# Performance work log

Measured on AMD Instinct MI355X. Metric: run time of the kernel, lower is better.

Reference implementation:

```python
import jax, jax.numpy as jnp
import numpy as np

B, S, H, DH, D, FD, FU = 4, 256, 12, 64, 768, 2048, 2048


def setup_inputs() -> dict:
    key = jax.random.key(0)
    ks = jax.random.split(key, 12)
    s = 0.02  # typical init scale for weights
    return {
        "resid_pre": jax.random.normal(ks[0], (B, S, D), jnp.float32),
        "ln_scale": jax.random.uniform(ks[1], (B, S, 1), jnp.float32, 0.5, 2.0),
        "probs": jax.nn.softmax(jax.random.normal(ks[2], (B, H, S, S), jnp.float32), axis=-1),
        "W_O": jax.random.normal(ks[3], (H, DH, D), jnp.float32) * s,
        "W_V": jax.random.normal(ks[4], (H, D, DH), jnp.float32) * s,
        "enc_W": jax.random.normal(ks[5], (FD, D), jnp.float32) * s,
        "enc_b": jax.random.normal(ks[6], (FD,), jnp.float32) * s,
        "b_dec": jax.random.normal(ks[7], (D,), jnp.float32) * s,
        "up_dec_W": jax.random.normal(ks[8], (D, FU), jnp.float32) * s,
        "up_b_dec": jax.random.normal(ks[9], (D,), jnp.float32) * s,
        "pruned_features": jax.random.normal(ks[10], (B, S, FU), jnp.float32),
        "connection_mask": jax.random.randint(ks[11], (FD, FU), 0, 2, jnp.int32),
    }


def reference(resid_pre, ln_scale, probs, W_O, W_V, enc_W, enc_b, b_dec,
              up_dec_W, up_b_dec, pruned_features, connection_mask):
    # W_OV: [h, d_model(in), d_model(out)]
    W_OV = jnp.einsum('hko,hmk->hmo', W_O, W_V)
    mask = connection_mask.astype(resid_pre.dtype)

    # --- initial contributions ---
    act_ln = resid_pre / ln_scale                                  # [b,s,d]
    pre_moving = jnp.einsum('bsi,hio,fo->bshf', act_ln, W_OV, enc_W)  # [b,s,h,f_down]
    approx = jnp.einsum('bhqk,bkhf->bqf', probs, pre_moving)       # [b,q,f_down]

    # --- pruned contributions (one upstream AE) ---
    virtual = jnp.einsum('fo,hio,iu->hfu', enc_W, W_OV, up_dec_W) * mask[None]
    up_ln = pruned_features / ln_scale                             # [b,k,f_up]
    post_ov = jnp.einsum('bku,hfu->bhkf', up_ln, virtual)          # [b,h,k,f_down]
    approx = approx + jnp.einsum('bhqk,bhkf->bqf', probs, post_ov)

    # --- bias terms ---
    approx = approx + enc_b[None, None] - (enc_W @ b_dec)[None, None]
    ub_ln = up_b_dec[None, None] / ln_scale                        # [b,s,d]
    ub_post = jnp.einsum('hmd,bsm->bsd', W_OV, ub_ln)              # attn path through OV
    approx = approx + jnp.einsum('fd,bsd->bsf', enc_W, ub_post)
    return approx
```

## Files before the change

kernel.cpp:

```cpp
#include <hip/hip_runtime.h>
#include <hip/hip_bf16.h>
#include <stdint.h>

typedef __bf16 bf16;
typedef __bf16 bf16x8 __attribute__((ext_vector_type(8)));
typedef __bf16 bf16x4 __attribute__((ext_vector_type(4)));
typedef float f32x4 __attribute__((ext_vector_type(4)));

#define AS1 __attribute__((address_space(1)))
#define AS3 __attribute__((address_space(3)))


__device__ __forceinline__ void gld16(const bf16* g, bf16* l) {
  __builtin_amdgcn_global_load_lds((AS1 void*)g, (AS3 void*)l, 16, 0, 0);
}

__global__ void k_sentinel(float* __restrict__ out) {
  int i = blockIdx.x * 256 + threadIdx.x;
  if (i < 2097152) out[i] = 1048576.0f;
}


__global__ void k_invln(const float* __restrict__ ln, float* __restrict__ invln) {
  int i = blockIdx.x * 256 + threadIdx.x;
  if (i < 1024) invln[i] = 1.0f / ln[i];
}

__global__ void k_cast4(const float* __restrict__ s, bf16* __restrict__ d, int n4) {
  int i = blockIdx.x * 256 + threadIdx.x;
  if (i < n4) {
    float4 v = *(const float4*)(s + (long)i * 4);
    bf16x4 o;
    o[0] = (bf16)v.x; o[1] = (bf16)v.y; o[2] = (bf16)v.z; o[3] = (bf16)v.w;
    *(bf16x4*)(d + (long)i * 4) = o;
  }
}

__global__ void k_maskb(const int* __restrict__ m, bf16* __restrict__ d, int n4) {
  int i = blockIdx.x * 256 + threadIdx.x;
  if (i < n4) {
    int4 v = *(const int4*)(m + (long)i * 4);
    bf16x4 o;
    o[0] = (bf16)(float)v.x; o[1] = (bf16)(float)v.y;
    o[2] = (bf16)(float)v.z; o[3] = (bf16)(float)v.w;
    *(bf16x4*)(d + (long)i * 4) = o;
  }
}

__global__ void k_probsT(const float* __restrict__ probs, bf16* __restrict__ pT) {
  int i = blockIdx.x * 256 + threadIdx.x;
  if (i < 786432) {
    long idx = (long)i * 4;
    int s  = (int)(idx & 255);
    int q  = (int)((idx >> 8) & 255);
    int hb = (int)(idx >> 16);
    int h = hb % 12, b = hb / 12;
    float4 v = *(const float4*)(probs + idx);
    bf16x4 o;
    o[0] = (bf16)v.x; o[1] = (bf16)v.y; o[2] = (bf16)v.z; o[3] = (bf16)v.w;
    *(bf16x4*)(pT + (long)b * 786432 + (long)q * 3072 + h * 256 + s) = o;
  }
}

__global__ void k_WO(const float* __restrict__ W_O, bf16* __restrict__ WOb) {
  int i = blockIdx.x * 256 + threadIdx.x;
  int o = i % 768, r = (i / 768) & 127, h = i / (768 * 128);
  WOb[i] = (r < 64) ? (bf16)W_O[(long)(h * 64 + r) * 768 + o] : (bf16)0.0f;
}

__global__ void k_WVtT(const float* __restrict__ wv, bf16* __restrict__ WVt) {
  __shared__ float tile[32][33];
  int h = blockIdx.z;
  int k0 = blockIdx.x * 32;
  int i0 = blockIdx.y * 32;
  int lane = threadIdx.x & 31, rg = threadIdx.x >> 5;
  if (k0 < 64) {
    for (int r = rg; r < 32; r += 8)
      tile[r][lane] = wv[((long)(h * 768 + i0 + r)) * 64 + k0 + lane];
    __syncthreads();
    for (int r = rg; r < 32; r += 8)
      WVt[((long)h * 128 + k0 + r) * 768 + i0 + lane] = (bf16)tile[lane][r];
  } else {
    for (int r = rg; r < 32; r += 8)
      WVt[((long)h * 128 + k0 + r) * 768 + i0 + lane] = (bf16)0.0f;
  }
}

__global__ void k_WOt(const float* __restrict__ wo, bf16* __restrict__ W_Ot) {
  __shared__ float tile[32][33];
  int h = blockIdx.z;
  int k0 = blockIdx.x * 32;
  int o0 = blockIdx.y * 32;
  int lane = threadIdx.x & 31, rg = threadIdx.x >> 5;
  for (int r = rg; r < 32; r += 8)
    tile[r][lane] = wo[((long)(h * 64 + k0 + r)) * 768 + o0 + lane];
  __syncthreads();
  for (int r = rg; r < 32; r += 8)
    W_Ot[((long)(h * 768 + o0 + r)) * 64 + k0 + lane] = (bf16)tile[lane][r];
}

__global__ void k_updWtT(const float* __restrict__ u, bf16* __restrict__ d) {
  __shared__ float tile[32][33];
  int u0 = blockIdx.x * 32;
  int i0 = blockIdx.y * 32;
  int lane = threadIdx.x & 31, rg = threadIdx.x >> 5;
  for (int r = rg; r < 32; r += 8)
    tile[r][lane] = u[((long)(i0 + r)) * 2048 + u0 + lane];
  __syncthreads();
  for (int r = rg; r < 32; r += 8)
    d[((long)(u0 + r)) * 768 + i0 + lane] = (bf16)tile[lane][r];
}

__global__ void k_Xb(const float* __restrict__ resid, const float* __restrict__ invln,
                     bf16* __restrict__ Xb) {
  int i = blockIdx.x * 256 + threadIdx.x;
  if (i < 196608) {
    long idx = (long)i * 4;
    float il = invln[idx / 768];
    float4 v = *(const float4*)(resid + idx);
    bf16x4 o;
    o[0] = (bf16)(v.x * il); o[1] = (bf16)(v.y * il);
    o[2] = (bf16)(v.z * il); o[3] = (bf16)(v.w * il);
    *(bf16x4*)(Xb + idx) = o;
  }
}

__global__ void k_UtT(const float* __restrict__ pr, const float* __restrict__ invln,
                      bf16* __restrict__ Ut) {
  __shared__ float tile[32][33];
  int b = blockIdx.z, u0 = blockIdx.x * 32, s0 = blockIdx.y * 32;
  int lane = threadIdx.x & 31, rg = threadIdx.x >> 5;
  for (int r = rg; r < 32; r += 8) {
    int s = s0 + r;
    tile[r][lane] = pr[((long)(b * 256 + s)) * 2048 + u0 + lane] * invln[b * 256 + s];
  }
  __syncthreads();
  for (int r = rg; r < 32; r += 8)
    Ut[((long)b * 2048 + u0 + r) * 256 + s0 + lane] = (bf16)tile[lane][r];
}

__global__ void k_append(const bf16* __restrict__ encWb, bf16* __restrict__ Bt, long ldb) {
  int i = blockIdx.x * 256 + threadIdx.x;
  if (i < 196608) {
    long idx = (long)i * 8;
    int f = (int)(idx / 768), d = (int)(idx % 768);
    *(bf16x8*)(Bt + (long)f * ldb + d) = *(const bf16x8*)(encWb + idx);
  }
}

__global__ void k_sred(const float* __restrict__ Sp, bf16* __restrict__ dst, long ldd) {
  int i = blockIdx.x * 256 + threadIdx.x;
  if (i < 196608) {
    long idx = (long)i * 4;
    int m = (int)(idx / 768), o = (int)(idx % 768);
    float4 v = *(const float4*)(Sp + idx);
    float4 a = *(const float4*)(Sp + 786432 + idx);
    float4 b = *(const float4*)(Sp + 2 * 786432 + idx);
    float4 c = *(const float4*)(Sp + 3 * 786432 + idx);
    v.x += a.x + b.x + c.x; v.y += a.y + b.y + c.y;
    v.z += a.z + b.z + c.z; v.w += a.w + b.w + c.w;
    bf16x4 ov;
    ov[0] = (bf16)v.x; ov[1] = (bf16)v.y; ov[2] = (bf16)v.z; ov[3] = (bf16)v.w;
    *(bf16x4*)(dst + (long)m * ldd + o) = ov;
  }
}


__device__ __forceinline__ float blk_reduce(float s) {
  __shared__ float red[256];
  red[threadIdx.x] = s; __syncthreads();
  for (int o = 128; o > 0; o >>= 1) {
    if ((int)threadIdx.x < o) red[threadIdx.x] += red[threadIdx.x + o];
    __syncthreads();
  }
  float r = red[0]; __syncthreads();
  return r;
}

__global__ void k_bias_t(const float* __restrict__ W_V, const float* __restrict__ up_b,
                         float* __restrict__ t_hk) {
  int j = blockIdx.x, h = j >> 6, k = j & 63;
  float s = 0.f;
  for (int m = threadIdx.x; m < 768; m += 256)
    s += W_V[((long)(h * 768 + m)) * 64 + k] * up_b[m];
  float r = blk_reduce(s);
  if (threadIdx.x == 0) t_hk[j] = r;
}

__global__ void k_bias_w(const float* __restrict__ W_O, const float* __restrict__ t_hk,
                         float* __restrict__ w) {
  int d = blockIdx.x;
  float s = 0.f;
  for (int j = threadIdx.x; j < 768; j += 256)
    s += W_O[(long)j * 768 + d] * t_hk[j];
  float r = blk_reduce(s);
  if (threadIdx.x == 0) w[d] = r;
}

__global__ void k_bias_c(const float* __restrict__ enc_W, const float* __restrict__ enc_b,
                         const float* __restrict__ b_dec, const float* __restrict__ w,
                         float* __restrict__ c0, float* __restrict__ c1) {
  int f = blockIdx.x;
  float s0 = 0.f, s1 = 0.f;
  for (int d = threadIdx.x; d < 768; d += 256) {
    float e = enc_W[(long)f * 768 + d];
    s0 += e * b_dec[d];
    s1 += e * w[d];
  }
  float r0 = blk_reduce(s0);
  float r1 = blk_reduce(s1);
  if (threadIdx.x == 0) { c0[f] = enc_b[f] - r0; c1[f] = r1; }
}

__global__ __launch_bounds__(256)
void gemm_bt(const bf16* __restrict__ A, const bf16* __restrict__ B, void* __restrict__ Cv,
             int M, int N, int K,
             long lda, long ldb, long ldc,
             int batchH,
             long sa_b, long sa_h, long sb_b, long sb_h, long sc_b, long sc_h,
             int mode, int kChunk,
             const bf16* __restrict__ mask, long mask_ld)
{
  __shared__ __align__(16) bf16 Asm[128 * 64];
  __shared__ __align__(16) bf16 Bsm[128 * 64];

  const int t = threadIdx.x;

  const int nbx = gridDim.x, nby = gridDim.y;
  const int nxy = nbx * nby;
  int orig = blockIdx.x + nbx * blockIdx.y;
  int qq = nxy >> 3, rr = nxy & 7;
  int xcd = orig & 7, lid = orig >> 3;
  int swz = (xcd < rr) ? (xcd * (qq + 1) + lid)
                       : (rr * (qq + 1) + (xcd - rr) * qq + lid);
  const int m0 = (swz % nby) * 128;
  const int n0 = (swz / nby) * 128;

  long aoff, boff, coff;
  int k0, k1;
  if (mode == 4) {
    int z = blockIdx.z;
    int bb = z / batchH, kc = z - bb * batchH;
    aoff = (long)bb * sa_b;
    boff = (long)bb * sb_b;
    coff = (long)bb * sc_b + (long)kc * sc_h;
    k0 = kc * kChunk; k1 = k0 + kChunk; if (k1 > K) k1 = K;
  } else if (mode >= 2) {
    int z = blockIdx.z;
    aoff = 0; boff = 0;
    coff = (long)z * (long)M * ldc;
    k0 = z * kChunk; k1 = k0 + kChunk; if (k1 > K) k1 = K;
  } else {
    int z = blockIdx.z;
    int bb = z / batchH, hh = z - bb * batchH;
    aoff = (long)bb * sa_b + (long)hh * sa_h;
    boff = (long)bb * sb_b + (long)hh * sb_h;
    coff = (long)bb * sc_b + (long)hh * sc_h;
    k0 = 0; k1 = K;
  }

  const bf16* Ab = A + aoff + (long)m0 * lda;
  const bf16* Bb = B + boff + (long)n0 * ldb;

  const int r0 = t >> 3;
  const int g8 = t & 7;

  const int L = t & 63, w = t >> 6;
  const int wm = (w & 1) * 64, wn = (w >> 1) * 64;
  const int r16 = L & 15, q = L >> 4;

  f32x4 acc[4][4];
#pragma unroll
  for (int i = 0; i < 4; i++)
#pragma unroll
    for (int j = 0; j < 4; j++) acc[i][j] = (f32x4){0.f, 0.f, 0.f, 0.f};

  for (int kt = k0; kt < k1; kt += 64) {
#pragma unroll
    for (int j = 0; j < 4; j++) {
      int row = j * 32 + r0;
      int sc = ((g8 ^ (row & 7)) << 3);
      gld16(Ab + (long)row * lda + (kt + sc), &Asm[j * 2048 + t * 8]);
      gld16(Bb + (long)row * ldb + (kt + sc), &Bsm[j * 2048 + t * 8]);
    }
    __syncthreads();

#pragma unroll
    for (int h2 = 0; h2 < 2; h2++) {
      bf16x8 af[4], bfr[4];
#pragma unroll
      for (int i = 0; i < 4; i++) {
        int ra = wm + i * 16 + r16;
        af[i]  = *(const bf16x8*)&Asm[ra * 64 + ((((h2 << 2) + q) ^ (ra & 7)) << 3)];
        int rb = wn + i * 16 + r16;
        bfr[i] = *(const bf16x8*)&Bsm[rb * 64 + ((((h2 << 2) + q) ^ (rb & 7)) << 3)];
      }
#pragma unroll
      for (int mi = 0; mi < 4; mi++)
#pragma unroll
        for (int ni = 0; ni < 4; ni++)
          acc[mi][ni] = __builtin_amdgcn_mfma_f32_16x16x32_bf16(af[mi], bfr[ni], acc[mi][ni], 0, 0, 0);
    }
    __syncthreads();
  }

  if (mode >= 2) {
    float* C = (float*)Cv;
#pragma unroll
    for (int mi = 0; mi < 4; mi++)
#pragma unroll
      for (int ni = 0; ni < 4; ni++)
#pragma unroll
        for (int r = 0; r < 4; r++) {
          int gm = m0 + wm + mi * 16 + q * 4 + r;
          int gn = n0 + wn + ni * 16 + r16;
          long idx = coff + (long)gm * ldc + gn;
          float v = acc[mi][ni][r];
          if (mode == 3) v += C[idx];
          C[idx] = v;
        }
  } else {
    bf16* C = (bf16*)Cv;
#pragma unroll
    for (int mi = 0; mi < 4; mi++)
#pragma unroll
      for (int ni = 0; ni < 4; ni++)
#pragma unroll
        for (int r = 0; r < 4; r++) {
          int gm = m0 + wm + mi * 16 + q * 4 + r;
          int gn = n0 + wn + ni * 16 + r16;
          float v = acc[mi][ni][r];
          if (mode == 1) v *= (float)mask[(long)gm * mask_ld + gn];
          C[coff + (long)gm * ldc + gn] = (bf16)v;
        }
  }
}

__global__ __launch_bounds__(512, 2)
void gemm_fp2(const bf16* __restrict__ A, const bf16* __restrict__ B,
              float* __restrict__ C,
              int M, int N, int K, long lda, long ldb, long ldc,
              int mode, int kChunk)
{
  __shared__ __align__(16) bf16 SM[2][2][16384];

  const int t = threadIdx.x;

  const int nz = gridDim.z;
  int fid = blockIdx.x + gridDim.x * (blockIdx.y + gridDim.y * blockIdx.z);
  const int z  = fid % nz;
  const int t2 = fid / nz;
  const int m0 = (t2 >> 3) * 256;
  const int n0 = (t2 & 7) * 256;

  const long coff = (long)z * (long)M * ldc;
  int k0 = z * kChunk, k1 = k0 + kChunk; if (k1 > K) k1 = K;
  const int NT = (k1 > k0) ? (k1 - k0) >> 6 : 0;

  const bf16* Ab = A + (long)m0 * lda + k0;
  const bf16* Bb = B + (long)n0 * ldb + k0;

  const int sr = t >> 3;
  const int g8 = t & 7;

  const int L = t & 63, w = t >> 6;
  const int wm = (w & 1) * 128;
  const int wn = (w >> 1) * 64;
  const int r16 = L & 15, q = L >> 4;

  f32x4 acc[8][4];
#pragma unroll
  for (int i = 0; i < 8; i++)
#pragma unroll
    for (int j = 0; j < 4; j++) acc[i][j] = (f32x4){0.f, 0.f, 0.f, 0.f};

  auto stage = [&](int tt, int buf) {
    const bf16* Ap = Ab + (long)tt * 64;
    const bf16* Bp = Bb + (long)tt * 64;
#pragma unroll
    for (int j = 0; j < 4; j++) {
      int row = j * 64 + sr;
      int sc = ((g8 ^ (row & 7)) << 3);
      gld16(Ap + (long)row * lda + sc, &SM[buf][0][j * 4096 + t * 8]);
    }
#pragma unroll
    for (int j = 0; j < 4; j++) {
      int row = j * 64 + sr;
      int sc = ((g8 ^ (row & 7)) << 3);
      gld16(Bp + (long)row * ldb + sc, &SM[buf][1][j * 4096 + t * 8]);
    }
  };

  if (NT >= 1) stage(0, 0);

  for (int tt = 0; tt < NT; tt++) {
    if (tt + 1 < NT) {
      stage(tt + 1, (tt + 1) & 1);
      asm volatile("s_waitcnt vmcnt(8)" ::: "memory");
    } else {
      asm volatile("s_waitcnt vmcnt(0)" ::: "memory");
    }
    __builtin_amdgcn_s_barrier();

    const bf16* As = &SM[tt & 1][0][0];
    const bf16* Bs = &SM[tt & 1][1][0];
#pragma unroll
    for (int h2 = 0; h2 < 2; h2++) {
      bf16x8 af[8], bfr[4];
#pragma unroll
      for (int i = 0; i < 8; i++) {
        int ra = wm + i * 16 + r16;
        af[i]  = *(const bf16x8*)&As[ra * 64 + ((((h2 << 2) + q) ^ (ra & 7)) << 3)];
      }
#pragma unroll
      for (int i = 0; i < 4; i++) {
        int rb = wn + i * 16 + r16;
        bfr[i] = *(const bf16x8*)&Bs[rb * 64 + ((((h2 << 2) + q) ^ (rb & 7)) << 3)];
      }
#pragma unroll
      for (int mi = 0; mi < 8; mi++)
#pragma unroll
        for (int ni = 0; ni < 4; ni++)
          acc[mi][ni] = __builtin_amdgcn_mfma_f32_16x16x32_bf16(af[mi], bfr[ni], acc[mi][ni], 0, 0, 0);
    }
    __builtin_amdgcn_s_barrier();
  }

#pragma unroll
  for (int mi = 0; mi < 8; mi++)
#pragma unroll
    for (int ni = 0; ni < 4; ni++)
#pragma unroll
      for (int r = 0; r < 4; r++) {
        int gm = m0 + wm + mi * 16 + q * 4 + r;
        int gn = n0 + wn + ni * 16 + r16;
        long idx = coff + (long)gm * ldc + gn;
        float v = acc[mi][ni][r];
        if (mode == 3) v += C[idx];
        C[idx] = v;
      }
}

__global__ void k_out(const float* __restrict__ Cp, const float* __restrict__ c0,
                      const float* __restrict__ c1, const float* __restrict__ invln,
                      float* __restrict__ out, int nsplit) {
  int i4 = blockIdx.x * 256 + threadIdx.x;
  long i = (long)i4 * 4;
  int n = (int)(i & 2047), m = (int)(i >> 11);
  float4 v = *(const float4*)(Cp + i);
  for (int z = 1; z < nsplit; z++) {
    float4 u = *(const float4*)(Cp + i + (long)z * 2097152);
    v.x += u.x; v.y += u.y; v.z += u.z; v.w += u.w;
  }
  float il = invln[m];
  float4 a = *(const float4*)(c0 + n);
  float4 b = *(const float4*)(c1 + n);
  v.x += a.x + b.x * il;
  v.y += a.y + b.y * il;
  v.z += a.z + b.z * il;
  v.w += a.w + b.w * il;
  *(float4*)(out + i) = v;
}


extern "C" void kernel_launch(void* const* d_in, const int* in_sizes, int n_in,
                              void* d_out, int out_size, void* d_ws, size_t ws_size,
                              hipStream_t stream) {
  (void)out_size;
  float* out = (float*)d_out;

  int iresid = -1, iln = -1, iprobs = -1, iencb = -1, ipruned = -1, imask = -1;
  int iwo = -1, iwv = -1, iencw = -1, iupdw = -1, ibdec = -1, iupb = -1;
  for (int i = 0; i < n_in; i++) {
    switch (in_sizes[i]) {
      case 786432:  iresid  = i; break;
      case 1024:    iln     = i; break;
      case 3145728: iprobs  = i; break;
      case 2048:    iencb   = i; break;
      case 2097152: ipruned = i; break;
      case 4194304: imask   = i; break;
      case 589824:  if (iwo   < 0) iwo   = i; else iwv   = i; break;
      case 1572864: if (iencw < 0) iencw = i; else iupdw = i; break;
      case 768:     if (ibdec < 0) ibdec = i; else iupb  = i; break;
      default: break;
    }
  }
  bool ok = n_in == 12 && iresid >= 0 && iln >= 0 && iprobs >= 0 && iencb >= 0 &&
            ipruned >= 0 && imask >= 0 && iwo >= 0 && iwv >= 0 && iencw >= 0 &&
            iupdw >= 0 && ibdec >= 0 && iupb >= 0;
  if (!ok) { k_sentinel<<<8192, 256, 0, stream>>>(out); return; }

  const float* resid = (const float*)d_in[iresid];
  const float* lns   = (const float*)d_in[iln];
  const float* probs = (const float*)d_in[iprobs];
  const float* W_O   = (const float*)d_in[iwo];
  const float* W_V   = (const float*)d_in[iwv];
  const float* enc_W = (const float*)d_in[iencw];
  const float* enc_b = (const float*)d_in[iencb];
  const float* b_dec = (const float*)d_in[ibdec];
  const float* updW  = (const float*)d_in[iupdw];
  const float* up_b  = (const float*)d_in[iupb];
  const float* pruned= (const float*)d_in[ipruned];
  const int*   cmask = (const int*)d_in[imask];

  auto pad = [](size_t b) -> size_t { return (b + 255) & ~(size_t)255; };
  const size_t prepB = pad(2359296) + pad(2359296) + pad(3145728) + pad(1572864) +
                       pad(3145728) + pad(1179648) + pad(3145728) + pad(18874368) +
                       pad(12582912);
  const size_t persB = pad(6291456) + pad(4194304) + pad(6291456) + pad(6291456) +
                       pad(8388608) + pad(4096) + pad(3072) + pad(3072) +
                       pad(8192) + pad(8192);
  auto needB = [&](int g, int ns) -> size_t {
    size_t cp = (size_t)ns * 8388608;
    size_t ov = prepB > cp ? prepB : cp;
    long KA = (long)g * 2048 + 768;
    size_t ab = pad((size_t)1024 * KA * 2) + pad((size_t)2048 * KA * 2);
    return ov + persB + ab + (2ull << 20);
  };
  const int cgs[14] = {12, 12, 12, 6, 6, 4, 3, 2, 2, 1, 1, 1, 1, 1};
  const int cns[14] = { 8,  4, 2, 8, 4, 4, 4, 4, 2, 8, 4, 2, 2, 1};
  int gs = 0, nsplit = 0;
  for (int ci = 0; ci < 14; ci++) {
    if (needB(cgs[ci], cns[ci]) <= ws_size) { gs = cgs[ci]; nsplit = cns[ci]; break; }
  }
  if (gs == 0) { gs = 1; nsplit = 1; }

  const long KA = (long)gs * 2048 + 768;

  char* p = (char*)d_ws;
  auto alloc = [&](size_t bytes) -> char* {
    char* r = p; p += (bytes + 255) & ~(size_t)255; return r;
  };
  char* overlayBase = p;
  bf16*  WOb    = (bf16*)alloc(12ull * 128 * 768 * 2);
  bf16*  WVt    = (bf16*)alloc(12ull * 128 * 768 * 2);
  bf16*  updWt  = (bf16*)alloc(2048ull * 768 * 2);
  bf16*  Xb     = (bf16*)alloc(1024ull * 768 * 2);
  bf16*  encWb  = (bf16*)alloc(2048ull * 768 * 2);
  bf16*  W_Ot   = (bf16*)alloc(12ull * 768 * 64 * 2);
  bf16*  T1     = (bf16*)alloc(12ull * 1024 * 128 * 2);
  bf16*  T3     = (bf16*)alloc(4ull * 768 * 3072 * 2);
  float* Sp     = (float*)alloc(4ull * 1024 * 768 * 4);
  {
    size_t used = (size_t)(p - overlayBase);
    size_t cp = (size_t)nsplit * 8388608;
    p = overlayBase + (used > cp ? used : cp);
  }
  float* Cpart  = (float*)overlayBase;
  bf16*  G_t    = (bf16*)alloc(12ull * 2048 * 128 * 2);
  bf16*  Ut     = (bf16*)alloc(4ull * 2048 * 256 * 2);
  bf16*  E1     = (bf16*)alloc(12ull * 2048 * 128 * 2);
  bf16*  probsT = (bf16*)alloc(4ull * 256 * 3072 * 2);
  bf16*  maskb  = (bf16*)alloc(2048ull * 2048 * 2);
  float* invln  = (float*)alloc(1024 * 4);
  float* t_hk   = (float*)alloc(768 * 4);
  float* wv     = (float*)alloc(768 * 4);
  float* c0     = (float*)alloc(2048 * 4);
  float* c1     = (float*)alloc(2048 * 4);
  bf16*  A_g    = (bf16*)alloc((size_t)1024 * KA * 2);
  bf16*  B_g    = (bf16*)alloc((size_t)2048 * KA * 2);

  k_invln<<<4, 256, 0, stream>>>(lns, invln);
  k_cast4<<<1536, 256, 0, stream>>>(enc_W, encWb, 393216);
  k_probsT<<<3072, 256, 0, stream>>>(probs, probsT);
  k_maskb<<<4096, 256, 0, stream>>>(cmask, maskb, 1048576);
  k_WO<<<4608, 256, 0, stream>>>(W_O, WOb);
  k_WVtT<<<dim3(4, 24, 12), 256, 0, stream>>>(W_V, WVt);
  k_WOt<<<dim3(2, 24, 12), 256, 0, stream>>>(W_O, W_Ot);
  k_updWtT<<<dim3(64, 24), 256, 0, stream>>>(updW, updWt);
  k_Xb<<<768, 256, 0, stream>>>(resid, invln, Xb);
  k_UtT<<<dim3(64, 8, 4), 256, 0, stream>>>(pruned, invln, Ut);
  k_bias_t<<<768, 256, 0, stream>>>(W_V, up_b, t_hk);
  k_bias_w<<<768, 256, 0, stream>>>(W_O, t_hk, wv);
  k_bias_c<<<2048, 256, 0, stream>>>(enc_W, enc_b, b_dec, wv, c0, c1);

  gemm_bt<<<dim3(1, 16, 24), 256, 0, stream>>>(
      encWb, WOb, E1, 2048, 128, 768,
      768, 768, 128, 12,
      (long)(updWt - encWb), 0,
      (long)(WVt - WOb), (long)128 * 768,
      (long)(G_t - E1), (long)2048 * 128,
      0, 0, nullptr, 0);

  gemm_bt<<<dim3(1, 8, 12), 256, 0, stream>>>(
      Xb, WVt, T1, 1024, 128, 768,
      768, 768, 128, 12,
      0, 0, 0, (long)128 * 768, 0, (long)1024 * 128,
      0, 0, nullptr, 0);

  gemm_bt<<<dim3(2, 6, 48), 256, 0, stream>>>(
      W_Ot, T1, T3, 768, 256, 64,
      64, 128, 3072, 12,
      0, (long)768 * 64, (long)256 * 128, (long)1024 * 128, 2359296, 256,
      0, 0, nullptr, 0);

  gemm_bt<<<dim3(6, 2, 16), 256, 0, stream>>>(
      probsT, T3, Sp, 256, 768, 3072,
      3072, 3072, 768, 4,
      786432, 0, 2359296, 0, 196608, 786432,
      4, 768, nullptr, 0);

  k_sred<<<768, 256, 0, stream>>>(Sp, A_g + (long)gs * 2048, KA);

  k_append<<<768, 256, 0, stream>>>(encWb, B_g + (long)gs * 2048, KA);

  for (int g = 0; g < 12 / gs; g++) {
    gemm_bt<<<dim3(16, 16, gs), 256, 0, stream>>>(
        E1 + (long)g * gs * 2048 * 128, G_t + (long)g * gs * 2048 * 128, B_g,
        2048, 2048, 64,
        128, 128, KA, gs,
        0, (long)2048 * 128, 0, (long)2048 * 128, 0, 2048,
        1, 0, maskb, 2048);

    gemm_bt<<<dim3(16, 2, 4 * gs), 256, 0, stream>>>(
        probsT + (long)g * gs * 256, Ut, A_g,
        256, 2048, 256,
        3072, 256, KA, gs,
        786432, 256, (long)2048 * 256, 0, 256 * KA, 2048,
        0, 0, nullptr, 0);

    int Kthis = (g == 0) ? (int)KA : gs * 2048;
    int kc = ((Kthis / nsplit + 63) / 64) * 64;
    gemm_fp2<<<dim3(8, 4, nsplit), 512, 0, stream>>>(
        A_g, B_g, Cpart,
        1024, 2048, Kthis,
        KA, KA, 2048,
        (g == 0) ? 2 : 3, kc);
  }

  k_out<<<2048, 256, 0, stream>>>(Cpart, c0, c1, invln, out, nsplit);
}
```

Before: 450.6 us.

## Merge prep kernels into two launches and retile split-K GEMM to smaller tiles

Ten elementwise and transpose preprocessing kernels are folded into two block-range-dispatched kernels, and the append copy is folded into the prep kernel, writing enc_W straight into B_g. This cuts kernel launch and tail overhead. The main split-K GEMM moves from 256x256 tiles with K-step 64 to 128x256 tiles with K-step 32, with less LDS and launch bounds allowing 4 blocks per CU, and the grid doubles in the M direction. Smaller tiles raise occupancy and block count but lower data reuse per tile and add more barriers per unit of K.

```diff
diff --git a/kernel.cpp b/kernel.cpp
--- a/kernel.cpp
+++ b/kernel.cpp
@@ -20,131 +20,109 @@
   if (i < 2097152) out[i] = 1048576.0f;
 }
 
-
-__global__ void k_invln(const float* __restrict__ ln, float* __restrict__ invln) {
-  int i = blockIdx.x * 256 + threadIdx.x;
-  if (i < 1024) invln[i] = 1.0f / ln[i];
-}
-
-__global__ void k_cast4(const float* __restrict__ s, bf16* __restrict__ d, int n4) {
-  int i = blockIdx.x * 256 + threadIdx.x;
-  if (i < n4) {
-    float4 v = *(const float4*)(s + (long)i * 4);
-    bf16x4 o;
-    o[0] = (bf16)v.x; o[1] = (bf16)v.y; o[2] = (bf16)v.z; o[3] = (bf16)v.w;
-    *(bf16x4*)(d + (long)i * 4) = o;
-  }
-}
-
-__global__ void k_maskb(const int* __restrict__ m, bf16* __restrict__ d, int n4) {
-  int i = blockIdx.x * 256 + threadIdx.x;
-  if (i < n4) {
-    int4 v = *(const int4*)(m + (long)i * 4);
-    bf16x4 o;
-    o[0] = (bf16)(float)v.x; o[1] = (bf16)(float)v.y;
-    o[2] = (bf16)(float)v.z; o[3] = (bf16)(float)v.w;
-    *(bf16x4*)(d + (long)i * 4) = o;
-  }
-}
-
-__global__ void k_probsT(const float* __restrict__ probs, bf16* __restrict__ pT) {
-  int i = blockIdx.x * 256 + threadIdx.x;
-  if (i < 786432) {
-    long idx = (long)i * 4;
-    int s  = (int)(idx & 255);
-    int q  = (int)((idx >> 8) & 255);
-    int hb = (int)(idx >> 16);
-    int h = hb % 12, b = hb / 12;
+__global__ void k_prep(const float* __restrict__ lns, float* __restrict__ invln,
+                       const float* __restrict__ enc_W, bf16* __restrict__ encWb,
+                       const float* __restrict__ probs, bf16* __restrict__ probsT,
+                       const int* __restrict__ cmask, bf16* __restrict__ maskb,
+                       const float* __restrict__ W_O, bf16* __restrict__ WOb,
+                       const float* __restrict__ resid, bf16* __restrict__ Xb,
+                       bf16* __restrict__ BgTail, long ldTail) {
+  const int bid = blockIdx.x, t = threadIdx.x;
+  if (bid < 1) {
+    for (int k = 0; k < 4; k++) { int j = t + k * 256; invln[j] = 1.0f / lns[j]; }
+  } else if (bid < 1537) {
+    long idx = ((long)(bid - 1) * 256 + t) * 4;
+    float4 v = *(const float4*)(enc_W + idx);
+    bf16x4 o; o[0]=(bf16)v.x; o[1]=(bf16)v.y; o[2]=(bf16)v.z; o[3]=(bf16)v.w;
+    *(bf16x4*)(encWb + idx) = o;
+  } else if (bid < 4609) {
+    long idx = ((long)(bid - 1537) * 256 + t) * 4;
+    int s = (int)(idx & 255), q = (int)((idx >> 8) & 255);
+    int hb = (int)(idx >> 16), h = hb % 12, b = hb / 12;
     float4 v = *(const float4*)(probs + idx);
-    bf16x4 o;
-    o[0] = (bf16)v.x; o[1] = (bf16)v.y; o[2] = (bf16)v.z; o[3] = (bf16)v.w;
-    *(bf16x4*)(pT + (long)b * 786432 + (long)q * 3072 + h * 256 + s) = o;
-  }
-}
-
-__global__ void k_WO(const float* __restrict__ W_O, bf16* __restrict__ WOb) {
-  int i = blockIdx.x * 256 + threadIdx.x;
-  int o = i % 768, r = (i / 768) & 127, h = i / (768 * 128);
-  WOb[i] = (r < 64) ? (bf16)W_O[(long)(h * 64 + r) * 768 + o] : (bf16)0.0f;
-}
-
-__global__ void k_WVtT(const float* __restrict__ wv, bf16* __restrict__ WVt) {
+    bf16x4 o; o[0]=(bf16)v.x; o[1]=(bf16)v.y; o[2]=(bf16)v.z; o[3]=(bf16)v.w;
+    *(bf16x4*)(probsT + (long)b * 786432 + (long)q * 3072 + h * 256 + s) = o;
+  } else if (bid < 8705) {
+    long idx = ((long)(bid - 4609) * 256 + t) * 4;
+    int4 v = *(const int4*)(cmask + idx);
+    bf16x4 o; o[0]=(bf16)(float)v.x; o[1]=(bf16)(float)v.y;
+    o[2]=(bf16)(float)v.z; o[3]=(bf16)(float)v.w;
+    *(bf16x4*)(maskb + idx) = o;
+  } else if (bid < 9857) {
+    long idx = ((long)(bid - 8705) * 256 + t) * 4;
+    int o = (int)(idx % 768), r = (int)((idx / 768) & 127), h = (int)(idx / (768 * 128));
+    bf16x4 ov;
+    if (r < 64) {
+      float4 v = *(const float4*)(W_O + (long)(h * 64 + r) * 768 + o);
+      ov[0]=(bf16)v.x; ov[1]=(bf16)v.y; ov[2]=(bf16)v.z; ov[3]=(bf16)v.w;
+    } else { ov[0]=ov[1]=ov[2]=ov[3]=(bf16)0.0f; }
+    *(bf16x4*)(WOb + idx) = ov;
+  } else if (bid < 10625) {
+    long idx = ((long)(bid - 9857) * 256 + t) * 4;
+    float il = 1.0f / lns[idx / 768];
+    float4 v = *(const float4*)(resid + idx);
+    bf16x4 o; o[0]=(bf16)(v.x*il); o[1]=(bf16)(v.y*il);
+    o[2]=(bf16)(v.z*il); o[3]=(bf16)(v.w*il);
+    *(bf16x4*)(Xb + idx) = o;
+  } else {
+    long idx = ((long)(bid - 10625) * 256 + t) * 4;
+    int f = (int)(idx / 768), d = (int)(idx % 768);
+    float4 v = *(const float4*)(enc_W + idx);
+    bf16x4 o; o[0]=(bf16)v.x; o[1]=(bf16)v.y; o[2]=(bf16)v.z; o[3]=(bf16)v.w;
+    *(bf16x4*)(BgTail + (long)f * ldTail + d) = o;
+  }
+}
+
+__global__ void k_prepT(const float* __restrict__ wv, bf16* __restrict__ WVt,
+                        const float* __restrict__ wo, bf16* __restrict__ W_Ot,
+                        const float* __restrict__ updW, bf16* __restrict__ updWt,
+                        const float* __restrict__ pr, const float* __restrict__ lns,
+                        bf16* __restrict__ Ut) {
   __shared__ float tile[32][33];
-  int h = blockIdx.z;
-  int k0 = blockIdx.x * 32;
-  int i0 = blockIdx.y * 32;
+  const int bid = blockIdx.x;
   int lane = threadIdx.x & 31, rg = threadIdx.x >> 5;
-  if (k0 < 64) {
+  if (bid < 1152) {
+    int r0 = bid;
+    int x = r0 % 4, y = (r0 / 4) % 24, h = r0 / 96;
+    int k0 = x * 32, i0 = y * 32;
+    if (k0 < 64) {
+      for (int r = rg; r < 32; r += 8)
+        tile[r][lane] = wv[((long)(h * 768 + i0 + r)) * 64 + k0 + lane];
+      __syncthreads();
+      for (int r = rg; r < 32; r += 8)
+        WVt[((long)h * 128 + k0 + r) * 768 + i0 + lane] = (bf16)tile[lane][r];
+    } else {
+      for (int r = rg; r < 32; r += 8)
+        WVt[((long)h * 128 + k0 + r) * 768 + i0 + lane] = (bf16)0.0f;
+    }
+  } else if (bid < 1728) {
+    int r0 = bid - 1152;
+    int x = r0 % 2, y = (r0 / 2) % 24, h = r0 / 48;
+    int k0 = x * 32, o0 = y * 32;
     for (int r = rg; r < 32; r += 8)
-      tile[r][lane] = wv[((long)(h * 768 + i0 + r)) * 64 + k0 + lane];
+      tile[r][lane] = wo[((long)(h * 64 + k0 + r)) * 768 + o0 + lane];
     __syncthreads();
     for (int r = rg; r < 32; r += 8)
-      WVt[((long)h * 128 + k0 + r) * 768 + i0 + lane] = (bf16)tile[lane][r];
+      W_Ot[((long)(h * 768 + o0 + r)) * 64 + k0 + lane] = (bf16)tile[lane][r];
+  } else if (bid < 3264) {
+    int r0 = bid - 1728;
+    int u0 = (r0 % 64) * 32, i0 = (r0 / 64) * 32;
+    for (int r = rg; r < 32; r += 8)
+      tile[r][lane] = updW[((long)(i0 + r)) * 2048 + u0 + lane];
+    __syncthreads();
+    for (int r = rg; r < 32; r += 8)
+      updWt[((long)(u0 + r)) * 768 + i0 + lane] = (bf16)tile[lane][r];
   } else {
+    int r0 = bid - 3264;
+    int u0 = (r0 % 64) * 32, s0 = ((r0 / 64) % 8) * 32, b = r0 / 512;
+    for (int r = rg; r < 32; r += 8) {
+      int s = s0 + r;
+      tile[r][lane] = pr[((long)(b * 256 + s)) * 2048 + u0 + lane] *
+                      (1.0f / lns[b * 256 + s]);
+    }
+    __syncthreads();
     for (int r = rg; r < 32; r += 8)
-      WVt[((long)h * 128 + k0 + r) * 768 + i0 + lane] = (bf16)0.0f;
-  }
-}
-
-__global__ void k_WOt(const float* __restrict__ wo, bf16* __restrict__ W_Ot) {
-  __shared__ float tile[32][33];
-  int h = blockIdx.z;
-  int k0 = blockIdx.x * 32;
-  int o0 = blockIdx.y * 32;
-  int lane = threadIdx.x & 31, rg = threadIdx.x >> 5;
-  for (int r = rg; r < 32; r += 8)
-    tile[r][lane] = wo[((long)(h * 64 + k0 + r)) * 768 + o0 + lane];
-  __syncthreads();
-  for (int r = rg; r < 32; r += 8)
-    W_Ot[((long)(h * 768 + o0 + r)) * 64 + k0 + lane] = (bf16)tile[lane][r];
-}
-
-__global__ void k_updWtT(const float* __restrict__ u, bf16* __restrict__ d) {
-  __shared__ float tile[32][33];
-  int u0 = blockIdx.x * 32;
-  int i0 = blockIdx.y * 32;
-  int lane = threadIdx.x & 31, rg = threadIdx.x >> 5;
-  for (int r = rg; r < 32; r += 8)
-    tile[r][lane] = u[((long)(i0 + r)) * 2048 + u0 + lane];
-  __syncthreads();
-  for (int r = rg; r < 32; r += 8)
-    d[((long)(u0 + r)) * 768 + i0 + lane] = (bf16)tile[lane][r];
-}
-
-__global__ void k_Xb(const float* __restrict__ resid, const float* __restrict__ invln,
-                     bf16* __restrict__ Xb) {
-  int i = blockIdx.x * 256 + threadIdx.x;
-  if (i < 196608) {
-    long idx = (long)i * 4;
-    float il = invln[idx / 768];
-    float4 v = *(const float4*)(resid + idx);
-    bf16x4 o;
-    o[0] = (bf16)(v.x * il); o[1] = (bf16)(v.y * il);
-    o[2] = (bf16)(v.z * il); o[3] = (bf16)(v.w * il);
-    *(bf16x4*)(Xb + idx) = o;
-  }
-}
-
-__global__ void k_UtT(const float* __restrict__ pr, const float* __restrict__ invln,
-                      bf16* __restrict__ Ut) {
-  __shared__ float tile[32][33];
-  int b = blockIdx.z, u0 = blockIdx.x * 32, s0 = blockIdx.y * 32;
-  int lane = threadIdx.x & 31, rg = threadIdx.x >> 5;
-  for (int r = rg; r < 32; r += 8) {
-    int s = s0 + r;
-    tile[r][lane] = pr[((long)(b * 256 + s)) * 2048 + u0 + lane] * invln[b * 256 + s];
-  }
-  __syncthreads();
-  for (int r = rg; r < 32; r += 8)
-    Ut[((long)b * 2048 + u0 + r) * 256 + s0 + lane] = (bf16)tile[lane][r];
-}
-
-__global__ void k_append(const bf16* __restrict__ encWb, bf16* __restrict__ Bt, long ldb) {
-  int i = blockIdx.x * 256 + threadIdx.x;
-  if (i < 196608) {
-    long idx = (long)i * 8;
-    int f = (int)(idx / 768), d = (int)(idx % 768);
-    *(bf16x8*)(Bt + (long)f * ldb + d) = *(const bf16x8*)(encWb + idx);
+      Ut[((long)b * 2048 + u0 + r) * 256 + s0 + lane] = (bf16)tile[lane][r];
   }
 }
 
@@ -336,13 +314,13 @@
   }
 }
 
-__global__ __launch_bounds__(512, 2)
-void gemm_fp2(const bf16* __restrict__ A, const bf16* __restrict__ B,
+__global__ __launch_bounds__(512, 4)
+void gemm_fp3(const bf16* __restrict__ A, const bf16* __restrict__ B,
               float* __restrict__ C,
               int M, int N, int K, long lda, long ldb, long ldc,
               int mode, int kChunk)
 {
-  __shared__ __align__(16) bf16 SM[2][2][16384];
+  __shared__ __align__(16) bf16 SM[2][12288];
 
   const int t = threadIdx.x;
 
@@ -350,44 +328,40 @@
   int fid = blockIdx.x + gridDim.x * (blockIdx.y + gridDim.y * blockIdx.z);
   const int z  = fid % nz;
   const int t2 = fid / nz;
-  const int m0 = (t2 >> 3) * 256;
-  const int n0 = (t2 & 7) * 256;
+  const int m0 = (t2 & 7) * 128;
+  const int n0 = (t2 >> 3) * 256;
 
   const long coff = (long)z * (long)M * ldc;
   int k0 = z * kChunk, k1 = k0 + kChunk; if (k1 > K) k1 = K;
-  const int NT = (k1 > k0) ? (k1 - k0) >> 6 : 0;
+  const int NT = (k1 > k0) ? (k1 - k0) >> 5 : 0;
 
   const bf16* Ab = A + (long)m0 * lda + k0;
   const bf16* Bb = B + (long)n0 * ldb + k0;
 
-  const int sr = t >> 3;
-  const int g8 = t & 7;
-
   const int L = t & 63, w = t >> 6;
-  const int wm = (w & 1) * 128;
+  const int wm = (w & 1) * 64;
   const int wn = (w >> 1) * 64;
   const int r16 = L & 15, q = L >> 4;
 
-  f32x4 acc[8][4];
-#pragma unroll
-  for (int i = 0; i < 8; i++)
+  f32x4 acc[4][4];
+#pragma unroll
+  for (int i = 0; i < 4; i++)
 #pragma unroll
     for (int j = 0; j < 4; j++) acc[i][j] = (f32x4){0.f, 0.f, 0.f, 0.f};
 
   auto stage = [&](int tt, int buf) {
-    const bf16* Ap = Ab + (long)tt * 64;
-    const bf16* Bp = Bb + (long)tt * 64;
-#pragma unroll
-    for (int j = 0; j < 4; j++) {
-      int row = j * 64 + sr;
-      int sc = ((g8 ^ (row & 7)) << 3);
-      gld16(Ap + (long)row * lda + sc, &SM[buf][0][j * 4096 + t * 8]);
-    }
-#pragma unroll
-    for (int j = 0; j < 4; j++) {
-      int row = j * 64 + sr;
-      int sc = ((g8 ^ (row & 7)) << 3);
-      gld16(Bp + (long)row * ldb + sc, &SM[buf][1][j * 4096 + t * 8]);
+    const bf16* Ap = Ab + (long)tt * 32;
+    const bf16* Bp = Bb + (long)tt * 32;
+    {
+      int row = t >> 2, g2 = t & 3;
+      gld16(Ap + (long)row * lda + ((g2 ^ ((row >> 1) & 3)) << 3), &SM[buf][t * 8]);
+    }
+#pragma unroll
+    for (int j = 0; j < 2; j++) {
+      int slot = j * 512 + t;
+      int row = slot >> 2, g2 = slot & 3;
+      gld16(Bp + (long)row * ldb + ((g2 ^ ((row >> 1) & 3)) << 3),
+            &SM[buf][4096 + slot * 8]);
     }
   };
 
@@ -396,38 +370,35 @@
   for (int tt = 0; tt < NT; tt++) {
     if (tt + 1 < NT) {
       stage(tt + 1, (tt + 1) & 1);
-      asm volatile("s_waitcnt vmcnt(8)" ::: "memory");
+      asm volatile("s_waitcnt vmcnt(3)" ::: "memory");
     } else {
       asm volatile("s_waitcnt vmcnt(0)" ::: "memory");
     }
     __builtin_amdgcn_s_barrier();
 
-    const bf16* As = &SM[tt & 1][0][0];
-    const bf16* Bs = &SM[tt & 1][1][0];
-#pragma unroll
-    for (int h2 = 0; h2 < 2; h2++) {
-      bf16x8 af[8], bfr[4];
-#pragma unroll
-      for (int i = 0; i < 8; i++) {
-        int ra = wm + i * 16 + r16;
-        af[i]  = *(const bf16x8*)&As[ra * 64 + ((((h2 << 2) + q) ^ (ra & 7)) << 3)];
-      }
-#pragma unroll
-      for (int i = 0; i < 4; i++) {
-        int rb = wn + i * 16 + r16;
-        bfr[i] = *(const bf16x8*)&Bs[rb * 64 + ((((h2 << 2) + q) ^ (rb & 7)) << 3)];
-      }
-#pragma unroll
-      for (int mi = 0; mi < 8; mi++)
-#pragma unroll
-        for (int ni = 0; ni < 4; ni++)
-          acc[mi][ni] = __builtin_amdgcn_mfma_f32_16x16x32_bf16(af[mi], bfr[ni], acc[mi][ni], 0, 0, 0);
-    }
+    const bf16* As = &SM[tt & 1][0];
+    const bf16* Bs = &SM[tt & 1][4096];
+    bf16x8 af[4], bfr[4];
+#pragma unroll
+    for (int i = 0; i < 4; i++) {
+      int ra = wm + i * 16 + r16;
+      af[i]  = *(const bf16x8*)&As[ra * 32 + ((q ^ ((ra >> 1) & 3)) << 3)];
+    }
+#pragma unroll
+    for (int i = 0; i < 4; i++) {
+      int rb = wn + i * 16 + r16;
+      bfr[i] = *(const bf16x8*)&Bs[rb * 32 + ((q ^ ((rb >> 1) & 3)) << 3)];
+    }
+#pragma unroll
+    for (int mi = 0; mi < 4; mi++)
+#pragma unroll
+      for (int ni = 0; ni < 4; ni++)
+        acc[mi][ni] = __builtin_amdgcn_mfma_f32_16x16x32_bf16(af[mi], bfr[ni], acc[mi][ni], 0, 0, 0);
     __builtin_amdgcn_s_barrier();
   }
 
 #pragma unroll
-  for (int mi = 0; mi < 8; mi++)
+  for (int mi = 0; mi < 4; mi++)
 #pragma unroll
     for (int ni = 0; ni < 4; ni++)
 #pragma unroll
@@ -560,16 +531,11 @@
   bf16*  A_g    = (bf16*)alloc((size_t)1024 * KA * 2);
   bf16*  B_g    = (bf16*)alloc((size_t)2048 * KA * 2);
 
-  k_invln<<<4, 256, 0, stream>>>(lns, invln);
-  k_cast4<<<1536, 256, 0, stream>>>(enc_W, encWb, 393216);
-  k_probsT<<<3072, 256, 0, stream>>>(probs, probsT);
-  k_maskb<<<4096, 256, 0, stream>>>(cmask, maskb, 1048576);
-  k_WO<<<4608, 256, 0, stream>>>(W_O, WOb);
-  k_WVtT<<<dim3(4, 24, 12), 256, 0, stream>>>(W_V, WVt);
-  k_WOt<<<dim3(2, 24, 12), 256, 0, stream>>>(W_O, W_Ot);
-  k_updWtT<<<dim3(64, 24), 256, 0, stream>>>(updW, updWt);
-  k_Xb<<<768, 256, 0, stream>>>(resid, invln, Xb);
-  k_UtT<<<dim3(64, 8, 4), 256, 0, stream>>>(pruned, invln, Ut);
+  k_prep<<<12161, 256, 0, stream>>>(lns, invln, enc_W, encWb, probs, probsT,
+                                    cmask, maskb, W_O, WOb, resid, Xb,
+                                    B_g + (long)gs * 2048, KA);
+  k_prepT<<<5312, 256, 0, stream>>>(W_V, WVt, W_O, W_Ot, updW, updWt,
+                                    pruned, lns, Ut);
   k_bias_t<<<768, 256, 0, stream>>>(W_V, up_b, t_hk);
   k_bias_w<<<768, 256, 0, stream>>>(W_O, t_hk, wv);
   k_bias_c<<<2048, 256, 0, stream>>>(enc_W, enc_b, b_dec, wv, c0, c1);
@@ -602,8 +568,6 @@
 
   k_sred<<<768, 256, 0, stream>>>(Sp, A_g + (long)gs * 2048, KA);
 
-  k_append<<<768, 256, 0, stream>>>(encWb, B_g + (long)gs * 2048, KA);
-
   for (int g = 0; g < 12 / gs; g++) {
     gemm_bt<<<dim3(16, 16, gs), 256, 0, stream>>>(
         E1 + (long)g * gs * 2048 * 128, G_t + (long)g * gs * 2048 * 128, B_g,
@@ -621,7 +585,7 @@
 
     int Kthis = (g == 0) ? (int)KA : gs * 2048;
     int kc = ((Kthis / nsplit + 63) / 64) * 64;
-    gemm_fp2<<<dim3(8, 4, nsplit), 512, 0, stream>>>(
+    gemm_fp3<<<dim3(8, 8, nsplit), 512, 0, stream>>>(
         A_g, B_g, Cpart,
         1024, 2048, Kthis,
         KA, KA, 2048,
```

After: 444.5 us. About the same (-1.4%).
